# Kernel optimization log

Measured on AMD Instinct MI355X. Metric: run time of the kernel, lower is better.

The kernel has to match this reference:

```python
import jax, jax.numpy as jnp
import numpy as np

K = 8        # num_caps
NITER = 3    # routing iterations per layer
NLAYER = 2   # number of NeibRoutLayer layers
TAU = 1.0
SLOPE = 0.01 # torch leaky_relu default
EPS = 1e-12  # torch F.normalize default eps


def capsnorm(v, k):
    # L2-normalize each of k capsule chunks along its delta_d axis.
    n, d = v.shape
    vk = v.reshape(n, k, d // k)
    nr = jnp.sqrt(jnp.sum(vk * vk, axis=2, keepdims=True))
    return (vk / jnp.maximum(nr, EPS)).reshape(n, d)


def rout(x, src, trg, k, niter, tau):
    n, d = x.shape
    dd = d // k
    x = capsnorm(x, k)
    z = x[src].reshape(-1, k, dd)  # [m, k, dd] neighbor capsules (constant over iters)
    u = x
    for _ in range(niter):
        # per-edge, per-capsule agreement score
        p = jnp.einsum('mkc,mkc->mk', z, u[trg].reshape(-1, k, dd))
        p = jax.nn.softmax(p / tau, axis=1)
        msg = (z * p[:, :, None]).reshape(-1, d)
        u = jax.ops.segment_sum(msg, trg, num_segments=n) + x
        u = capsnorm(u, k)
    return u


def setup_inputs() -> dict:
    key = jax.random.key(0)
    k1, k2, k3, k4 = jax.random.split(key, 4)
    n, m, in_dim, hid = 50000, 500000, 500, 64
    x = jax.random.normal(k1, (n, in_dim), dtype=jnp.float32)
    src_trg = jax.random.randint(k2, (2, m), 0, n)
    stdv = 1.0 / np.sqrt(hid)  # SparseInputLinear.reset_parameters
    W = jax.random.uniform(k3, (in_dim, hid), minval=-stdv, maxval=stdv, dtype=jnp.float32)
    b = jax.random.uniform(k4, (hid,), minval=-stdv, maxval=stdv, dtype=jnp.float32)
    return {"x": x, "src_trg": src_trg, "W": W, "b": b}


def reference(x, src_trg, W, b):
    # eval mode: dropout(p=0.0, training=False) is identity
    src, trg = src_trg[0], src_trg[1]
    h = jax.nn.leaky_relu(x @ W + b, negative_slope=SLOPE)
    for _ in range(NLAYER):
        h = jax.nn.leaky_relu(rout(h, src, trg, K, NITER, TAU), negative_slope=SLOPE)
    return h
```

## Files before the change

kernel.cpp:

```cpp
#include <hip/hip_runtime.h>
#include <hip/hip_bf16.h>

static constexpr float SLOPE = 0.01f;
static constexpr float EPSN  = 1e-12f;

typedef float f32x4 __attribute__((ext_vector_type(4)));
typedef short short8 __attribute__((ext_vector_type(8)));

#define KPAD 512
#define CAP  16

template <int CTRL>
__device__ __forceinline__ float dpp_add(float x) {
  const int y = __builtin_amdgcn_mov_dpp(__builtin_bit_cast(int, x), CTRL, 0xF, 0xF, true);
  return x + __builtin_bit_cast(float, y);
}

__device__ __forceinline__ void bf16_split(float v, short& hi, short& lo) {
  __hip_bfloat16 h = __float2bfloat16(v);
  float hf = __bfloat162float(h);
  __hip_bfloat16 l = __float2bfloat16(v - hf);
  hi = __builtin_bit_cast(short, h);
  lo = __builtin_bit_cast(short, l);
}

__device__ __forceinline__ void load_lds16(const float* g, float* l) {
  __builtin_amdgcn_global_load_lds(
      (const __attribute__((address_space(1))) unsigned int*)g,
      (__attribute__((address_space(3))) unsigned int*)l, 16, 0, 0);
}

__global__ __launch_bounds__(256) void prep_w_k(const float* __restrict__ W,
                                                short* __restrict__ w2h,
                                                short* __restrict__ w2l,
                                                float* __restrict__ zbuf, int in_dim) {
  const int idx = blockIdx.x * 256 + threadIdx.x;
  if (idx < 4) zbuf[idx] = 0.0f;
  if (idx >= KPAD * 64) return;
  const int k = idx >> 6, col = idx & 63;
  const float v = (k < in_dim) ? W[(size_t)k * 64 + col] : 0.0f;
  short hi, lo;
  bf16_split(v, hi, lo);
  const int kt = k >> 5, kc = (k >> 3) & 3, e = k & 7;
  const int off = (((kt * 4 + kc) * 64) + col) * 8 + e;
  w2h[off] = hi;
  w2l[off] = lo;
}

__device__ __forceinline__ void stage_tile(const float* __restrict__ x,
                                           const float* __restrict__ zbuf,
                                           float* ldsbuf, int row0w, int kt,
                                           int n, int in_dim, int lane) {
  const int rl = lane >> 4;
  const int gl = lane & 15;
#pragma unroll
  for (int i = 0; i < 4; ++i) {
    const int r    = i * 4 + rl;
    const int gsrc = gl ^ (r & 7);
    const int k    = kt * 64 + gsrc * 4;
    int grow = row0w + r;
    grow = grow < n ? grow : n - 1;
    const float* src = (k + 4 <= in_dim) ? (x + (size_t)grow * in_dim + k) : zbuf;
    load_lds16(src, ldsbuf + i * 256);
  }
}

__global__ __launch_bounds__(256) void gemm_mfma_capsnorm_k(
    const float* __restrict__ x, const short* __restrict__ w2h,
    const short* __restrict__ w2l, const float* __restrict__ b,
    const float* __restrict__ zbuf, float* __restrict__ xn, int n, int in_dim) {
  __shared__ __align__(16) float xs[4][2][1024];

  const int tid   = threadIdx.x;
  const int lane  = tid & 63;
  const int w     = tid >> 6;
  const int l15   = lane & 15;
  const int kcL   = lane >> 4;
  const int row0  = blockIdx.x * 64;
  const int row0w = row0 + w * 16;
  const int sw4   = l15 & 7;

  f32x4 acc0 = {0.f, 0.f, 0.f, 0.f};
  f32x4 acc1 = {0.f, 0.f, 0.f, 0.f};
  f32x4 acc2 = {0.f, 0.f, 0.f, 0.f};
  f32x4 acc3 = {0.f, 0.f, 0.f, 0.f};

  stage_tile(x, zbuf, &xs[w][0][0], row0w, 0, n, in_dim, lane);

  for (int kt = 0; kt < 8; ++kt) {
    float* cur = &xs[w][kt & 1][0];
    float* nxt = &xs[w][(kt & 1) ^ 1][0];

    const int s00 = ((kcL * 2)     ^ sw4) * 4;
    const int s01 = ((kcL * 2 + 1) ^ sw4) * 4;
    const int s10 = ((8 + kcL * 2)     ^ sw4) * 4;
    const int s11 = ((8 + kcL * 2 + 1) ^ sw4) * 4;
    const float4 fa0 = *reinterpret_cast<const float4*>(&cur[l15 * 64 + s00]);
    const float4 fb0 = *reinterpret_cast<const float4*>(&cur[l15 * 64 + s01]);
    const float4 fa1 = *reinterpret_cast<const float4*>(&cur[l15 * 64 + s10]);
    const float4 fb1 = *reinterpret_cast<const float4*>(&cur[l15 * 64 + s11]);

    if (kt < 7) stage_tile(x, zbuf, nxt, row0w, kt + 1, n, in_dim, lane);

#pragma unroll
    for (int ks = 0; ks < 2; ++ks) {
      const float4 A0 = ks ? fa1 : fa0;
      const float4 A1 = ks ? fb1 : fb0;
      short hb[8], lb[8];
      bf16_split(A0.x, hb[0], lb[0]);
      bf16_split(A0.y, hb[1], lb[1]);
      bf16_split(A0.z, hb[2], lb[2]);
      bf16_split(A0.w, hb[3], lb[3]);
      bf16_split(A1.x, hb[4], lb[4]);
      bf16_split(A1.y, hb[5], lb[5]);
      bf16_split(A1.z, hb[6], lb[6]);
      bf16_split(A1.w, hb[7], lb[7]);
      const short8 ah = *reinterpret_cast<const short8*>(hb);
      const short8 al = *reinterpret_cast<const short8*>(lb);
      const int ktg = kt * 2 + ks;
      const size_t base = ((size_t)(ktg * 4 + kcL) * 64) * 8;
#pragma unroll
      for (int nt = 0; nt < 4; ++nt) {
        const short8 bh = *reinterpret_cast<const short8*>(w2h + base + (size_t)(nt * 16 + l15) * 8);
        const short8 bl = *reinterpret_cast<const short8*>(w2l + base + (size_t)(nt * 16 + l15) * 8);
        f32x4& acc = nt == 0 ? acc0 : nt == 1 ? acc1 : nt == 2 ? acc2 : acc3;
        acc = __builtin_amdgcn_mfma_f32_16x16x32_bf16(ah, bh, acc, 0, 0, 0);
        acc = __builtin_amdgcn_mfma_f32_16x16x32_bf16(ah, bl, acc, 0, 0, 0);
        acc = __builtin_amdgcn_mfma_f32_16x16x32_bf16(al, bh, acc, 0, 0, 0);
      }
    }
  }

#pragma unroll
  for (int nt = 0; nt < 4; ++nt) {
    const f32x4 acc = nt == 0 ? acc0 : nt == 1 ? acc1 : nt == 2 ? acc2 : acc3;
    const float bcol = b[nt * 16 + l15];
#pragma unroll
    for (int reg = 0; reg < 4; ++reg) {
      float v = acc[reg] + bcol;
      v = v > 0.f ? v : SLOPE * v;
      float s = v * v;
      s = dpp_add<0xB1>(s);
      s = dpp_add<0x4E>(s);
      s += __shfl_xor(s, 4);
      const float inv = 1.0f / fmaxf(sqrtf(s), EPSN);
      const int grow = row0 + w * 16 + ((lane >> 4) << 2) + reg;
      if (grow < n) xn[(size_t)grow * 64 + nt * 16 + l15] = v * inv;
    }
  }
}

__global__ __launch_bounds__(256) void zero_int_k(int* __restrict__ p, int n) {
  const int i = blockIdx.x * blockDim.x + threadIdx.x;
  if (i < n) p[i] = 0;
}

__global__ __launch_bounds__(256) void hist_k(const int* __restrict__ trg,
                                              int* __restrict__ counts, int m) {
  const int e = blockIdx.x * blockDim.x + threadIdx.x;
  if (e < m) atomicAdd(&counts[trg[e]], 1);
}

__global__ __launch_bounds__(256) void scanA_k(const int* __restrict__ counts,
                                               int* __restrict__ bsum, int n) {
  const int i = blockIdx.x * 256 + threadIdx.x;
  int v = (i < n) ? counts[i] : 0;
  v += __shfl_xor(v, 1);  v += __shfl_xor(v, 2);  v += __shfl_xor(v, 4);
  v += __shfl_xor(v, 8);  v += __shfl_xor(v, 16); v += __shfl_xor(v, 32);
  __shared__ int wsum[4];
  if ((threadIdx.x & 63) == 0) wsum[threadIdx.x >> 6] = v;
  __syncthreads();
  if (threadIdx.x == 0) bsum[blockIdx.x] = wsum[0] + wsum[1] + wsum[2] + wsum[3];
}

__global__ __launch_bounds__(256) void scanB_k(int* __restrict__ bsum, int nblk,
                                               int* __restrict__ row_ptr, int n, int m) {
  const int i = threadIdx.x;
  const int lane = i & 63;
  const int wave = i >> 6;
  const int v = (i < nblk) ? bsum[i] : 0;
  int inc = v;
#pragma unroll
  for (int d = 1; d < 64; d <<= 1) {
    int t = __shfl_up(inc, d);
    if (lane >= d) inc += t;
  }
  __shared__ int wsum[4];
  if (lane == 63) wsum[wave] = inc;
  __syncthreads();
  int base = 0;
  for (int q = 0; q < wave; ++q) base += wsum[q];
  if (i < nblk) bsum[i] = base + inc - v;
  if (i == 0) row_ptr[n] = m;
}

__global__ __launch_bounds__(256) void scanC_k(const int* __restrict__ counts,
                                               const int* __restrict__ bsum,
                                               int* __restrict__ row_ptr,
                                               int* __restrict__ cursor, int n) {
  const int i = blockIdx.x * 256 + threadIdx.x;
  const int lane = threadIdx.x & 63;
  const int wave = threadIdx.x >> 6;
  const int v = (i < n) ? counts[i] : 0;
  int inc = v;
#pragma unroll
  for (int d = 1; d < 64; d <<= 1) {
    int t = __shfl_up(inc, d);
    if (lane >= d) inc += t;
  }
  __shared__ int wsum[4];
  if (lane == 63) wsum[wave] = inc;
  __syncthreads();
  int base = bsum[blockIdx.x];
  for (int q = 0; q < wave; ++q) base += wsum[q];
  const int excl = base + inc - v;
  if (i < n) { row_ptr[i] = excl; cursor[i] = excl; }
}

__global__ __launch_bounds__(256) void scatter_k(const int* __restrict__ src,
                                                 const int* __restrict__ trg,
                                                 int* __restrict__ cursor,
                                                 int* __restrict__ src_sorted, int m) {
  const int e = blockIdx.x * blockDim.x + threadIdx.x;
  if (e < m) {
    const int pos = atomicAdd(&cursor[trg[e]], 1);
    src_sorted[pos] = src[e];
  }
}

template <int MODE>
__global__ __launch_bounds__(256) void rout_layer_k(
    const int* __restrict__ row_ptr, const int* __restrict__ src_sorted,
    const float* __restrict__ xn, float* __restrict__ dst, int n) {
  __shared__ float zc[4][CAP * 64];
  const int wv   = threadIdx.x >> 6;
  const int wid  = blockIdx.x * 4 + wv;
  const int lane = threadIdx.x & 63;
  if (wid >= n) return;
  const int g = lane >> 4;
  const int q = lane & 15;
  const size_t rowj = (size_t)wid * 64 + q * 4;
  float* zbase = &zc[wv][0];

  const float4 xj = *reinterpret_cast<const float4*>(xn + rowj);
  float u0 = xj.x, u1 = xj.y, u2 = xj.z, u3 = xj.w;

  const int e0  = row_ptr[wid];
  const int end = row_ptr[wid + 1];
  const int ntile = (end - e0 + 3) >> 2;

  for (int t = 0; t < 3; ++t) {
    float a0 = 0.f, a1 = 0.f, a2 = 0.f, a3 = 0.f;

#define EDGE_BODY(Z)                                                   \
    {                                                                  \
      float d = (Z).x * u0;                                            \
      d = fmaf((Z).y, u1, d);                                          \
      d = fmaf((Z).z, u2, d);                                          \
      d = fmaf((Z).w, u3, d);                                          \
      d = dpp_add<0xB1>(d);                     \
      const float ee = __expf(d);           \
      float sm = dpp_add<0x4E>(ee);          \
      sm = dpp_add<0x124>(sm);               \
      sm = dpp_add<0x128>(sm);               \
      const float wgt = ee * __builtin_amdgcn_rcpf(sm);                \
      a0 = fmaf((Z).x, wgt, a0);                                       \
      a1 = fmaf((Z).y, wgt, a1);                                       \
      a2 = fmaf((Z).z, wgt, a2);                                       \
      a3 = fmaf((Z).w, wgt, a3);                                       \
    }

    if (t == 0) {
      int e = e0 + g;
      bool vn = e < end;
      int  sn = vn ? src_sorted[e] : wid;
      float4 zn = *reinterpret_cast<const float4*>(xn + (size_t)sn * 64 + q * 4);
      if (!vn) zn = make_float4(0.f, 0.f, 0.f, 0.f);
      for (int it = 0; it < ntile; ++it) {
        const float4 z = zn;
        e += 4;
        const bool v2 = e < end;
        const int  s2 = v2 ? src_sorted[e] : wid;
        float4 tz = *reinterpret_cast<const float4*>(xn + (size_t)s2 * 64 + q * 4);
        zn = v2 ? tz : make_float4(0.f, 0.f, 0.f, 0.f);
        const int slot = it * 4 + g;
        if (slot < CAP)
          *reinterpret_cast<float4*>(zbase + slot * 64 + q * 4) = z;
        EDGE_BODY(z)
      }
    } else {
      for (int it = 0; it < ntile; ++it) {
        const int slot = it * 4 + g;
        float4 z;
        if (slot < CAP) {
          z = *reinterpret_cast<const float4*>(zbase + slot * 64 + q * 4);
        } else {
          const int e = e0 + slot;
          const bool vv = e < end;
          const int ss = vv ? src_sorted[e] : wid;
          z = *reinterpret_cast<const float4*>(xn + (size_t)ss * 64 + q * 4);
          if (!vv) z = make_float4(0.f, 0.f, 0.f, 0.f);
        }
        EDGE_BODY(z)
      }
    }
#undef EDGE_BODY

    a0 += __shfl_xor(a0, 16); a0 += __shfl_xor(a0, 32);
    a1 += __shfl_xor(a1, 16); a1 += __shfl_xor(a1, 32);
    a2 += __shfl_xor(a2, 16); a2 += __shfl_xor(a2, 32);
    a3 += __shfl_xor(a3, 16); a3 += __shfl_xor(a3, 32);
    a0 += xj.x; a1 += xj.y; a2 += xj.z; a3 += xj.w;
    float ss = a0 * a0 + a1 * a1 + a2 * a2 + a3 * a3;
    ss = dpp_add<0xB1>(ss);
    const float inv = 1.0f / fmaxf(sqrtf(ss), EPSN);
    u0 = a0 * inv; u1 = a1 * inv; u2 = a2 * inv; u3 = a3 * inv;
  }

  float v0 = u0, v1 = u1, v2 = u2, v3 = u3;
  v0 = v0 > 0.f ? v0 : SLOPE * v0;
  v1 = v1 > 0.f ? v1 : SLOPE * v1;
  v2 = v2 > 0.f ? v2 : SLOPE * v2;
  v3 = v3 > 0.f ? v3 : SLOPE * v3;
  if (MODE == 1) {
    float s3 = v0 * v0 + v1 * v1 + v2 * v2 + v3 * v3;
    s3 = dpp_add<0xB1>(s3);
    const float inv3 = 1.0f / fmaxf(sqrtf(s3), EPSN);
    v0 *= inv3; v1 *= inv3; v2 *= inv3; v3 *= inv3;
  }
  if (g == 0) {
    *reinterpret_cast<float4*>(dst + rowj) = make_float4(v0, v1, v2, v3);
  }
}

extern "C" void kernel_launch(void* const* d_in, const int* in_sizes, int n_in,
                              void* d_out, int out_size, void* d_ws, size_t ws_size,
                              hipStream_t stream) {
  const float* x       = (const float*)d_in[0];
  const int*   src_trg = (const int*)d_in[1];
  const float* W       = (const float*)d_in[2];
  const float* b       = (const float*)d_in[3];

  const int hid    = in_sizes[3];
  const int in_dim = in_sizes[2] / hid;
  const int n      = in_sizes[0] / in_dim;
  const int m      = in_sizes[1] / 2;
  const int* src = src_trg;
  const int* trg = src_trg + m;

  const size_t n64 = (size_t)n * hid;
  float* xn_a = (float*)d_ws;
  float* xn_b = xn_a + n64;
  short* w2h  = (short*)(xn_b + n64);
  short* w2l  = w2h + KPAD * 64;
  float* zbuf = (float*)(w2l + KPAD * 64);
  int*   ip   = (int*)(zbuf + 4);
  int* counts     = ip;
  int* row_ptr    = counts + n;
  int* cursor     = row_ptr + n + 1;
  int* bsum       = cursor + n;
  const int nblk  = (n + 255) / 256;
  int* src_sorted = bsum + nblk;
  float* out = (float*)d_out;

  const int mg = (m + 255) / 256;

  zero_int_k<<<nblk, 256, 0, stream>>>(counts, n);
  hist_k<<<mg, 256, 0, stream>>>(trg, counts, m);
  scanA_k<<<nblk, 256, 0, stream>>>(counts, bsum, n);
  scanB_k<<<1, 256, 0, stream>>>(bsum, nblk, row_ptr, n, m);
  scanC_k<<<nblk, 256, 0, stream>>>(counts, bsum, row_ptr, cursor, n);
  scatter_k<<<mg, 256, 0, stream>>>(src, trg, cursor, src_sorted, m);

  prep_w_k<<<(KPAD * 64) / 256, 256, 0, stream>>>(W, w2h, w2l, zbuf, in_dim);
  gemm_mfma_capsnorm_k<<<(n + 63) / 64, 256, 0, stream>>>(
      x, w2h, w2l, b, zbuf, xn_a, n, in_dim);

  const int rb = (n + 3) / 4;
  rout_layer_k<1><<<rb, 256, 0, stream>>>(row_ptr, src_sorted, xn_a, xn_b, n);
  rout_layer_k<2><<<rb, 256, 0, stream>>>(row_ptr, src_sorted, xn_b, out, n);
}
```

Measured before the change: 169.8 us.

## Remap routing kernel to one lane per capsule, eight edges per wave

Each lane now owns one full 8-float capsule instead of a 4-float half, so a wave handles 8 edges per step instead of 4. The per-capsule dot product is computed in registers without a cross-lane add. The softmax over the 8 capsules uses three DPP steps across 8 lanes. This halves the number of edge-loop iterations per node and removes a DPP reduction per edge. In exchange each lane holds more registers, nodes with few edges leave more lanes idle as padding, and the final accumulator reduction grows to a DPP step plus two shuffles per element.

```diff
diff --git a/kernel.cpp b/kernel.cpp
--- a/kernel.cpp
+++ b/kernel.cpp
@@ -237,99 +237,122 @@
   const int wid  = blockIdx.x * 4 + wv;
   const int lane = threadIdx.x & 63;
   if (wid >= n) return;
-  const int g = lane >> 4;
-  const int q = lane & 15;
-  const size_t rowj = (size_t)wid * 64 + q * 4;
+  const int g = lane >> 3;
+  const int c = lane & 7;
+  const size_t rowj = (size_t)wid * 64 + c * 8;
   float* zbase = &zc[wv][0];
 
-  const float4 xj = *reinterpret_cast<const float4*>(xn + rowj);
-  float u0 = xj.x, u1 = xj.y, u2 = xj.z, u3 = xj.w;
+  const float4 xa = *reinterpret_cast<const float4*>(xn + rowj);
+  const float4 xbv = *reinterpret_cast<const float4*>(xn + rowj + 4);
+  float u[8] = {xa.x, xa.y, xa.z, xa.w, xbv.x, xbv.y, xbv.z, xbv.w};
 
   const int e0  = row_ptr[wid];
   const int end = row_ptr[wid + 1];
-  const int ntile = (end - e0 + 3) >> 2;
+  const int ntile = (end - e0 + 7) >> 3;
 
   for (int t = 0; t < 3; ++t) {
-    float a0 = 0.f, a1 = 0.f, a2 = 0.f, a3 = 0.f;
-
-#define EDGE_BODY(Z)                                                   \
+    float a[8] = {0.f, 0.f, 0.f, 0.f, 0.f, 0.f, 0.f, 0.f};
+
+#define EDGE_BODY(ZA, ZB)                                              \
     {                                                                  \
-      float d = (Z).x * u0;                                            \
-      d = fmaf((Z).y, u1, d);                                          \
-      d = fmaf((Z).z, u2, d);                                          \
-      d = fmaf((Z).w, u3, d);                                          \
-      d = dpp_add<0xB1>(d);                     \
+      float d = (ZA).x * u[0];                                         \
+      d = fmaf((ZA).y, u[1], d);                                       \
+      d = fmaf((ZA).z, u[2], d);                                       \
+      d = fmaf((ZA).w, u[3], d);                                       \
+      d = fmaf((ZB).x, u[4], d);                                       \
+      d = fmaf((ZB).y, u[5], d);                                       \
+      d = fmaf((ZB).z, u[6], d);                                       \
+      d = fmaf((ZB).w, u[7], d);        \
       const float ee = __expf(d);           \
-      float sm = dpp_add<0x4E>(ee);          \
-      sm = dpp_add<0x124>(sm);               \
-      sm = dpp_add<0x128>(sm);               \
+      float sm = dpp_add<0xB1>(ee);                          \
+      sm = dpp_add<0x4E>(sm);                                \
+      sm = dpp_add<0x141>(sm);               \
       const float wgt = ee * __builtin_amdgcn_rcpf(sm);                \
-      a0 = fmaf((Z).x, wgt, a0);                                       \
-      a1 = fmaf((Z).y, wgt, a1);                                       \
-      a2 = fmaf((Z).z, wgt, a2);                                       \
-      a3 = fmaf((Z).w, wgt, a3);                                       \
+      a[0] = fmaf((ZA).x, wgt, a[0]);                                  \
+      a[1] = fmaf((ZA).y, wgt, a[1]);                                  \
+      a[2] = fmaf((ZA).z, wgt, a[2]);                                  \
+      a[3] = fmaf((ZA).w, wgt, a[3]);                                  \
+      a[4] = fmaf((ZB).x, wgt, a[4]);                                  \
+      a[5] = fmaf((ZB).y, wgt, a[5]);                                  \
+      a[6] = fmaf((ZB).z, wgt, a[6]);                                  \
+      a[7] = fmaf((ZB).w, wgt, a[7]);                                  \
     }
 
     if (t == 0) {
       int e = e0 + g;
       bool vn = e < end;
       int  sn = vn ? src_sorted[e] : wid;
-      float4 zn = *reinterpret_cast<const float4*>(xn + (size_t)sn * 64 + q * 4);
-      if (!vn) zn = make_float4(0.f, 0.f, 0.f, 0.f);
+      float4 zna = *reinterpret_cast<const float4*>(xn + (size_t)sn * 64 + c * 8);
+      float4 znb = *reinterpret_cast<const float4*>(xn + (size_t)sn * 64 + c * 8 + 4);
+      if (!vn) { zna = make_float4(0.f,0.f,0.f,0.f); znb = make_float4(0.f,0.f,0.f,0.f); }
       for (int it = 0; it < ntile; ++it) {
-        const float4 z = zn;
-        e += 4;
+        const float4 za = zna, zb = znb;
+        e += 8;
         const bool v2 = e < end;
         const int  s2 = v2 ? src_sorted[e] : wid;
-        float4 tz = *reinterpret_cast<const float4*>(xn + (size_t)s2 * 64 + q * 4);
-        zn = v2 ? tz : make_float4(0.f, 0.f, 0.f, 0.f);
-        const int slot = it * 4 + g;
-        if (slot < CAP)
-          *reinterpret_cast<float4*>(zbase + slot * 64 + q * 4) = z;
-        EDGE_BODY(z)
+        float4 ta = *reinterpret_cast<const float4*>(xn + (size_t)s2 * 64 + c * 8);
+        float4 tb = *reinterpret_cast<const float4*>(xn + (size_t)s2 * 64 + c * 8 + 4);
+        zna = v2 ? ta : make_float4(0.f,0.f,0.f,0.f);
+        znb = v2 ? tb : make_float4(0.f,0.f,0.f,0.f);
+        const int slot = it * 8 + g;
+        if (slot < CAP) {
+          *reinterpret_cast<float4*>(zbase + slot * 64 + c * 8)     = za;
+          *reinterpret_cast<float4*>(zbase + slot * 64 + c * 8 + 4) = zb;
+        }
+        EDGE_BODY(za, zb)
       }
     } else {
       for (int it = 0; it < ntile; ++it) {
-        const int slot = it * 4 + g;
-        float4 z;
+        const int slot = it * 8 + g;
+        float4 za, zb;
         if (slot < CAP) {
-          z = *reinterpret_cast<const float4*>(zbase + slot * 64 + q * 4);
+          za = *reinterpret_cast<const float4*>(zbase + slot * 64 + c * 8);
+          zb = *reinterpret_cast<const float4*>(zbase + slot * 64 + c * 8 + 4);
         } else {
           const int e = e0 + slot;
           const bool vv = e < end;
           const int ss = vv ? src_sorted[e] : wid;
-          z = *reinterpret_cast<const float4*>(xn + (size_t)ss * 64 + q * 4);
-          if (!vv) z = make_float4(0.f, 0.f, 0.f, 0.f);
+          za = *reinterpret_cast<const float4*>(xn + (size_t)ss * 64 + c * 8);
+          zb = *reinterpret_cast<const float4*>(xn + (size_t)ss * 64 + c * 8 + 4);
+          if (!vv) { za = make_float4(0.f,0.f,0.f,0.f); zb = make_float4(0.f,0.f,0.f,0.f); }
         }
-        EDGE_BODY(z)
+        EDGE_BODY(za, zb)
       }
     }
 #undef EDGE_BODY
 
-    a0 += __shfl_xor(a0, 16); a0 += __shfl_xor(a0, 32);
-    a1 += __shfl_xor(a1, 16); a1 += __shfl_xor(a1, 32);
-    a2 += __shfl_xor(a2, 16); a2 += __shfl_xor(a2, 32);
-    a3 += __shfl_xor(a3, 16); a3 += __shfl_xor(a3, 32);
-    a0 += xj.x; a1 += xj.y; a2 += xj.z; a3 += xj.w;
-    float ss = a0 * a0 + a1 * a1 + a2 * a2 + a3 * a3;
-    ss = dpp_add<0xB1>(ss);
+#pragma unroll
+    for (int k = 0; k < 8; ++k) {
+      a[k] = dpp_add<0x128>(a[k]);
+      a[k] += __shfl_xor(a[k], 16);
+      a[k] += __shfl_xor(a[k], 32);
+    }
+    a[0] += xa.x; a[1] += xa.y; a[2] += xa.z; a[3] += xa.w;
+    a[4] += xbv.x; a[5] += xbv.y; a[6] += xbv.z; a[7] += xbv.w;
+    float ss = a[0]*a[0];
+#pragma unroll
+    for (int k = 1; k < 8; ++k) ss = fmaf(a[k], a[k], ss);
     const float inv = 1.0f / fmaxf(sqrtf(ss), EPSN);
-    u0 = a0 * inv; u1 = a1 * inv; u2 = a2 * inv; u3 = a3 * inv;
-  }
-
-  float v0 = u0, v1 = u1, v2 = u2, v3 = u3;
-  v0 = v0 > 0.f ? v0 : SLOPE * v0;
-  v1 = v1 > 0.f ? v1 : SLOPE * v1;
-  v2 = v2 > 0.f ? v2 : SLOPE * v2;
-  v3 = v3 > 0.f ? v3 : SLOPE * v3;
+#pragma unroll
+    for (int k = 0; k < 8; ++k) u[k] = a[k] * inv;
+  }
+
+  float v[8];
+#pragma unroll
+  for (int k = 0; k < 8; ++k) {
+    v[k] = u[k] > 0.f ? u[k] : SLOPE * u[k];
+  }
   if (MODE == 1) {
-    float s3 = v0 * v0 + v1 * v1 + v2 * v2 + v3 * v3;
-    s3 = dpp_add<0xB1>(s3);
+    float s3 = v[0]*v[0];
+#pragma unroll
+    for (int k = 1; k < 8; ++k) s3 = fmaf(v[k], v[k], s3);
     const float inv3 = 1.0f / fmaxf(sqrtf(s3), EPSN);
-    v0 *= inv3; v1 *= inv3; v2 *= inv3; v3 *= inv3;
+#pragma unroll
+    for (int k = 0; k < 8; ++k) v[k] *= inv3;
   }
   if (g == 0) {
-    *reinterpret_cast<float4*>(dst + rowj) = make_float4(v0, v1, v2, v3);
+    *reinterpret_cast<float4*>(dst + rowj)     = make_float4(v[0], v[1], v[2], v[3]);
+    *reinterpret_cast<float4*>(dst + rowj + 4) = make_float4(v[4], v[5], v[6], v[7]);
   }
 }
 
```

After: 181.2 us. +6.7%, slower.

## Keep first 16 neighbor capsules in registers and merge scan kernels

Applied to the files above, without the earlier changes.

The routing kernel drops the per-wave LDS cache of neighbor capsules and instead loads the first 16 edges' capsule vectors into registers before the routing iterations. Edges beyond 16 are re-gathered from global memory on every iteration. Separately, the three-kernel prefix scan is replaced by a single-block serial-chunk scan, and the zeroing kernel is replaced with hipMemsetAsync, cutting launch count. The single-block scan has each thread read about 200 counts serially, which may be slower than the parallel version, and holding the capsules in registers raises register pressure.

```diff
diff --git a/kernel.cpp b/kernel.cpp
--- a/kernel.cpp
+++ b/kernel.cpp
@@ -8,7 +8,6 @@
 typedef short short8 __attribute__((ext_vector_type(8)));
 
 #define KPAD 512
-#define CAP  16
 
 template <int CTRL>
 __device__ __forceinline__ float dpp_add(float x) {
@@ -150,36 +149,24 @@
   }
 }
 
-__global__ __launch_bounds__(256) void zero_int_k(int* __restrict__ p, int n) {
-  const int i = blockIdx.x * blockDim.x + threadIdx.x;
-  if (i < n) p[i] = 0;
-}
-
 __global__ __launch_bounds__(256) void hist_k(const int* __restrict__ trg,
                                               int* __restrict__ counts, int m) {
   const int e = blockIdx.x * blockDim.x + threadIdx.x;
   if (e < m) atomicAdd(&counts[trg[e]], 1);
 }
 
-__global__ __launch_bounds__(256) void scanA_k(const int* __restrict__ counts,
-                                               int* __restrict__ bsum, int n) {
-  const int i = blockIdx.x * 256 + threadIdx.x;
-  int v = (i < n) ? counts[i] : 0;
-  v += __shfl_xor(v, 1);  v += __shfl_xor(v, 2);  v += __shfl_xor(v, 4);
-  v += __shfl_xor(v, 8);  v += __shfl_xor(v, 16); v += __shfl_xor(v, 32);
-  __shared__ int wsum[4];
-  if ((threadIdx.x & 63) == 0) wsum[threadIdx.x >> 6] = v;
-  __syncthreads();
-  if (threadIdx.x == 0) bsum[blockIdx.x] = wsum[0] + wsum[1] + wsum[2] + wsum[3];
-}
-
-__global__ __launch_bounds__(256) void scanB_k(int* __restrict__ bsum, int nblk,
-                                               int* __restrict__ row_ptr, int n, int m) {
-  const int i = threadIdx.x;
-  const int lane = i & 63;
-  const int wave = i >> 6;
-  const int v = (i < nblk) ? bsum[i] : 0;
-  int inc = v;
+__global__ __launch_bounds__(256) void scan_all_k(const int* __restrict__ counts,
+                                                  int* __restrict__ row_ptr,
+                                                  int* __restrict__ cursor,
+                                                  int n, int m) {
+  const int tid   = threadIdx.x;
+  const int chunk = (n + 255) / 256;
+  const int lo = tid * chunk;
+  const int hi = min(lo + chunk, n);
+  int sum = 0;
+  for (int i = lo; i < hi; ++i) sum += counts[i];
+  const int lane = tid & 63, wave = tid >> 6;
+  int inc = sum;
 #pragma unroll
   for (int d = 1; d < 64; d <<= 1) {
     int t = __shfl_up(inc, d);
@@ -190,31 +177,14 @@
   __syncthreads();
   int base = 0;
   for (int q = 0; q < wave; ++q) base += wsum[q];
-  if (i < nblk) bsum[i] = base + inc - v;
-  if (i == 0) row_ptr[n] = m;
-}
-
-__global__ __launch_bounds__(256) void scanC_k(const int* __restrict__ counts,
-                                               const int* __restrict__ bsum,
-                                               int* __restrict__ row_ptr,
-                                               int* __restrict__ cursor, int n) {
-  const int i = blockIdx.x * 256 + threadIdx.x;
-  const int lane = threadIdx.x & 63;
-  const int wave = threadIdx.x >> 6;
-  const int v = (i < n) ? counts[i] : 0;
-  int inc = v;
-#pragma unroll
-  for (int d = 1; d < 64; d <<= 1) {
-    int t = __shfl_up(inc, d);
-    if (lane >= d) inc += t;
-  }
-  __shared__ int wsum[4];
-  if (lane == 63) wsum[wave] = inc;
-  __syncthreads();
-  int base = bsum[blockIdx.x];
-  for (int q = 0; q < wave; ++q) base += wsum[q];
-  const int excl = base + inc - v;
-  if (i < n) { row_ptr[i] = excl; cursor[i] = excl; }
+  int run = base + inc - sum;
+  for (int i = lo; i < hi; ++i) {
+    const int c = counts[i];
+    row_ptr[i] = run;
+    cursor[i]  = run;
+    run += c;
+  }
+  if (tid == 0) row_ptr[n] = m;
 }
 
 __global__ __launch_bounds__(256) void scatter_k(const int* __restrict__ src,
@@ -232,15 +202,13 @@
 __global__ __launch_bounds__(256) void rout_layer_k(
     const int* __restrict__ row_ptr, const int* __restrict__ src_sorted,
     const float* __restrict__ xn, float* __restrict__ dst, int n) {
-  __shared__ float zc[4][CAP * 64];
-  const int wv   = threadIdx.x >> 6;
-  const int wid  = blockIdx.x * 4 + wv;
+  const int wid  = blockIdx.x * 4 + (threadIdx.x >> 6);
   const int lane = threadIdx.x & 63;
   if (wid >= n) return;
   const int g = lane >> 4;
   const int q = lane & 15;
   const size_t rowj = (size_t)wid * 64 + q * 4;
-  float* zbase = &zc[wv][0];
+  const float4 fz = make_float4(0.f, 0.f, 0.f, 0.f);
 
   const float4 xj = *reinterpret_cast<const float4*>(xn + rowj);
   float u0 = xj.x, u1 = xj.y, u2 = xj.z, u3 = xj.w;
@@ -248,6 +216,21 @@
   const int e0  = row_ptr[wid];
   const int end = row_ptr[wid + 1];
   const int ntile = (end - e0 + 3) >> 2;
+
+  const int eA = e0 + g, eB = eA + 4, eC = eA + 8, eD = eA + 12;
+  const bool vA = eA < end, vB = eB < end, vC = eC < end, vD = eD < end;
+  const int iA = vA ? src_sorted[eA] : wid;
+  const int iB = vB ? src_sorted[eB] : wid;
+  const int iC = vC ? src_sorted[eC] : wid;
+  const int iD = vD ? src_sorted[eD] : wid;
+  float4 zA = *reinterpret_cast<const float4*>(xn + (size_t)iA * 64 + q * 4);
+  float4 zB = *reinterpret_cast<const float4*>(xn + (size_t)iB * 64 + q * 4);
+  float4 zC = *reinterpret_cast<const float4*>(xn + (size_t)iC * 64 + q * 4);
+  float4 zD = *reinterpret_cast<const float4*>(xn + (size_t)iD * 64 + q * 4);
+  if (!vA) zA = fz;
+  if (!vB) zB = fz;
+  if (!vC) zC = fz;
+  if (!vD) zD = fz;
 
   for (int t = 0; t < 3; ++t) {
     float a0 = 0.f, a1 = 0.f, a2 = 0.f, a3 = 0.f;
@@ -270,39 +253,17 @@
       a3 = fmaf((Z).w, wgt, a3);                                       \
     }
 
-    if (t == 0) {
-      int e = e0 + g;
-      bool vn = e < end;
-      int  sn = vn ? src_sorted[e] : wid;
-      float4 zn = *reinterpret_cast<const float4*>(xn + (size_t)sn * 64 + q * 4);
-      if (!vn) zn = make_float4(0.f, 0.f, 0.f, 0.f);
-      for (int it = 0; it < ntile; ++it) {
-        const float4 z = zn;
-        e += 4;
-        const bool v2 = e < end;
-        const int  s2 = v2 ? src_sorted[e] : wid;
-        float4 tz = *reinterpret_cast<const float4*>(xn + (size_t)s2 * 64 + q * 4);
-        zn = v2 ? tz : make_float4(0.f, 0.f, 0.f, 0.f);
-        const int slot = it * 4 + g;
-        if (slot < CAP)
-          *reinterpret_cast<float4*>(zbase + slot * 64 + q * 4) = z;
-        EDGE_BODY(z)
-      }
-    } else {
-      for (int it = 0; it < ntile; ++it) {
-        const int slot = it * 4 + g;
-        float4 z;
-        if (slot < CAP) {
-          z = *reinterpret_cast<const float4*>(zbase + slot * 64 + q * 4);
-        } else {
-          const int e = e0 + slot;
-          const bool vv = e < end;
-          const int ss = vv ? src_sorted[e] : wid;
-          z = *reinterpret_cast<const float4*>(xn + (size_t)ss * 64 + q * 4);
-          if (!vv) z = make_float4(0.f, 0.f, 0.f, 0.f);
-        }
-        EDGE_BODY(z)
-      }
+    EDGE_BODY(zA)
+    EDGE_BODY(zB)
+    EDGE_BODY(zC)
+    EDGE_BODY(zD)
+    for (int it = 4; it < ntile; ++it) {
+      const int e = e0 + it * 4 + g;
+      const bool vv = e < end;
+      const int ss = vv ? src_sorted[e] : wid;
+      float4 z = *reinterpret_cast<const float4*>(xn + (size_t)ss * 64 + q * 4);
+      if (!vv) z = fz;
+      EDGE_BODY(z)
     }
 #undef EDGE_BODY
 
@@ -358,18 +319,14 @@
   int* counts     = ip;
   int* row_ptr    = counts + n;
   int* cursor     = row_ptr + n + 1;
-  int* bsum       = cursor + n;
-  const int nblk  = (n + 255) / 256;
-  int* src_sorted = bsum + nblk;
+  int* src_sorted = cursor + n;
   float* out = (float*)d_out;
 
   const int mg = (m + 255) / 256;
 
-  zero_int_k<<<nblk, 256, 0, stream>>>(counts, n);
+  hipMemsetAsync(counts, 0, (size_t)n * sizeof(int), stream);
   hist_k<<<mg, 256, 0, stream>>>(trg, counts, m);
-  scanA_k<<<nblk, 256, 0, stream>>>(counts, bsum, n);
-  scanB_k<<<1, 256, 0, stream>>>(bsum, nblk, row_ptr, n, m);
-  scanC_k<<<nblk, 256, 0, stream>>>(counts, bsum, row_ptr, cursor, n);
+  scan_all_k<<<1, 256, 0, stream>>>(counts, row_ptr, cursor, n, m);
   scatter_k<<<mg, 256, 0, stream>>>(src, trg, cursor, src_sorted, m);
 
   prep_w_k<<<(KPAD * 64) / 256, 256, 0, stream>>>(W, w2h, w2l, zbuf, in_dim);
```

New measurement: 276.1 us. 62.6% more time.
